# Kernel tuning notes

Measured on AMD Instinct MI355X. Metric: run time of the kernel, lower is better.

Reference implementation:

```python
import jax, jax.numpy as jnp
import numpy as np

N = 50000   # nodes
E = 800000  # edges per graph
FD = 128    # input feature dim (sc and fc)
H = 128     # hidden_dim
G = 64      # graphs in batch
C = 2       # num_classes


def _sage(x, src, dst, Wl, Wr, b, n):
    # PyG SAGEConv (mean aggr): lin_l(mean_{j->i} x_j) + lin_r(x_i); bias lives in lin_l.
    msum = jax.ops.segment_sum(x[src], dst, num_segments=n)          # [n, F]
    cnt = jax.ops.segment_sum(jnp.ones((src.shape[0],), x.dtype), dst, num_segments=n)
    mean = msum / jnp.maximum(cnt, 1.0)[:, None]
    return mean @ Wl.T + x @ Wr.T + b


def setup_inputs() -> dict:
    key = jax.random.key(0)
    ks = jax.random.split(key, 24)
    s = 0.05
    inp = {
        "sc_x": jax.random.normal(ks[0], (N, FD), jnp.float32),
        "fc_x": jax.random.normal(ks[1], (N, FD), jnp.float32),
        "sc_edge_index": jax.random.randint(ks[2], (2, E), 0, N),
        "fc_edge_index": jax.random.randint(ks[3], (2, E), 0, N),
        "batch": jnp.sort(jax.random.randint(ks[4], (N,), 0, G)),
        # sc convs
        "sc_Wl1": jax.random.normal(ks[5], (H, FD), jnp.float32) * s,
        "sc_Wr1": jax.random.normal(ks[6], (H, FD), jnp.float32) * s,
        "sc_b1": jnp.zeros((H,), jnp.float32),
        "sc_Wl2": jax.random.normal(ks[7], (H, H), jnp.float32) * s,
        "sc_Wr2": jax.random.normal(ks[8], (H, H), jnp.float32) * s,
        "sc_b2": jnp.zeros((H,), jnp.float32),
        # fc convs
        "fc_Wl1": jax.random.normal(ks[9], (H, FD), jnp.float32) * s,
        "fc_Wr1": jax.random.normal(ks[10], (H, FD), jnp.float32) * s,
        "fc_b1": jnp.zeros((H,), jnp.float32),
        "fc_Wl2": jax.random.normal(ks[11], (H, H), jnp.float32) * s,
        "fc_Wr2": jax.random.normal(ks[12], (H, H), jnp.float32) * s,
        "fc_b2": jnp.zeros((H,), jnp.float32),
        # MLP head
        "W1": jax.random.normal(ks[13], (H, 2 * H), jnp.float32) * s,
        "bh1": jnp.zeros((H,), jnp.float32),
        "W2": jax.random.normal(ks[14], (H // 2, H), jnp.float32) * s,
        "bh2": jnp.zeros((H // 2,), jnp.float32),
        "W3": jax.random.normal(ks[15], (C, H // 2), jnp.float32) * s,
        "bh3": jnp.zeros((C,), jnp.float32),
    }
    return inp


def reference(sc_x, fc_x, sc_edge_index, fc_edge_index, batch,
              sc_Wl1, sc_Wr1, sc_b1, sc_Wl2, sc_Wr2, sc_b2,
              fc_Wl1, fc_Wr1, fc_b1, fc_Wl2, fc_Wr2, fc_b2,
              W1, bh1, W2, bh2, W3, bh3):
    # edge_index[0] = source j, edge_index[1] = target i (PyG convention)
    sc_src, sc_dst = sc_edge_index[0], sc_edge_index[1]
    fc_src, fc_dst = fc_edge_index[0], fc_edge_index[1]

    h = jax.nn.relu(_sage(sc_x, sc_src, sc_dst, sc_Wl1, sc_Wr1, sc_b1, N))
    h = jax.nn.relu(_sage(h, sc_src, sc_dst, sc_Wl2, sc_Wr2, sc_b2, N))
    sc_pool = jax.ops.segment_sum(h, batch, num_segments=G)  # global_add_pool -> [G, H]

    g = jax.nn.relu(_sage(fc_x, fc_src, fc_dst, fc_Wl1, fc_Wr1, fc_b1, N))
    g = jax.nn.relu(_sage(g, fc_src, fc_dst, fc_Wl2, fc_Wr2, fc_b2, N))
    fc_pool = jax.ops.segment_sum(g, batch, num_segments=G)  # [G, H]

    x = jnp.concatenate([sc_pool, fc_pool], axis=1)          # [G, 2H]
    # dropout is identity in eval mode
    x = jax.nn.relu(x @ W1.T + bh1)
    x = jax.nn.relu(x @ W2.T + bh2)
    return jax.nn.log_softmax(x @ W3.T + bh3, axis=-1)       # [G, C]
```

## Files before the change

### kernel.cpp

```cpp
#include <hip/hip_runtime.h>
#include <hip/hip_bf16.h>

#define N_NODES 50000
#define E_EDGES 800000
#define G_GRAPHS 64
#define NBUCK 392
#define BCAP 5120
#define NF ((size_t)N_NODES * 128)

typedef __attribute__((ext_vector_type(8))) short s16x8;
typedef __attribute__((ext_vector_type(4))) float f32x4;

constexpr size_t O_POOL   = 0;
constexpr size_t O_GCUR   = 16384;
constexpr size_t O_BSTART = 16896;
constexpr size_t O_ROW    = 17408;
constexpr size_t O_CNT    = 117408;
constexpr size_t O_ES     = 217408;
constexpr size_t O_WB     = 1817408;
constexpr size_t O_XB     = 1882944;
constexpr size_t O_MEAN   = 8282944;
constexpr size_t O_HB     = 14682944;
constexpr size_t ZERO_BYTES = (16384 + 512) * 4;

__device__ __forceinline__ unsigned short f2bf(float f) {
    __hip_bfloat16 h = __float2bfloat16(f);
    return *reinterpret_cast<unsigned short*>(&h);
}
__device__ __forceinline__ float bflo(unsigned int v) { return __uint_as_float(v << 16); }
__device__ __forceinline__ float bfhi(unsigned int v) { return __uint_as_float(v & 0xffff0000u); }

__global__ void __launch_bounds__(512) bin_pass1(const int* __restrict__ sc_e,
                                                 const int* __restrict__ fc_e,
                                                 int* __restrict__ gcur,
                                                 unsigned int* __restrict__ buf) {
    __shared__ int hcnt[512];
    __shared__ int hexcl[512];
    __shared__ int hcur[512];
    __shared__ int gbase[512];
    __shared__ int wsum[8];
    __shared__ unsigned int stage[4096];

    const int tid = threadIdx.x;
    const int lane = tid & 63;
    const int wid = tid >> 6;
    const int tile0 = blockIdx.x * 4096;

    hcnt[tid] = 0;
    __syncthreads();

    int eb[8];
    unsigned int pk[8];
    #pragma unroll
    for (int j = 0; j < 8; ++j) {
        int ec = tile0 + j * 512 + tid;
        if (ec < 2 * E_EDGES) {
            int set = (ec >= E_EDGES);
            int local = ec - set * E_EDGES;
            const int* ep = set ? fc_e : sc_e;
            int src = ep[local];
            int dst = ep[E_EDGES + local];
            eb[j] = set * 196 + (dst >> 8);
            pk[j] = ((unsigned int)(dst & 255) << 16) | (unsigned int)src;
            atomicAdd(&hcnt[eb[j]], 1);
        } else eb[j] = -1;
    }
    __syncthreads();

    {
        int v = hcnt[tid];
        int incl = v;
        #pragma unroll
        for (int d = 1; d < 64; d <<= 1) {
            int u = __shfl_up(incl, d, 64);
            if (lane >= d) incl += u;
        }
        if (lane == 63) wsum[wid] = incl;
        __syncthreads();
        int pre = 0;
        for (int w = 0; w < wid; ++w) pre += wsum[w];
        int excl = incl - v + pre;
        hexcl[tid] = excl;
        hcur[tid] = excl;
    }
    __syncthreads();

    if (tid < NBUCK) {
        int c = hcnt[tid];
        gbase[tid] = c ? atomicAdd(&gcur[tid], c) : 0;
    }

    #pragma unroll
    for (int j = 0; j < 8; ++j) {
        if (eb[j] >= 0) {
            int pos = atomicAdd(&hcur[eb[j]], 1);
            stage[pos] = pk[j];
        }
    }
    __syncthreads();

    for (int b = wid; b < NBUCK; b += 8) {
        int c = hcnt[b];
        if (!c) continue;
        int s = hexcl[b];
        int g0 = gbase[b];
        for (int i = lane; i < c; i += 64) {
            int gi = g0 + i;
            if (gi < BCAP) buf[(size_t)b * BCAP + gi] = stage[s + i];
        }
    }
}

__global__ void bstart_scan(const int* __restrict__ gcur, int* __restrict__ bstart) {
    __shared__ int wsum[8];
    int t = threadIdx.x;
    int lane = t & 63, wid = t >> 6;
    int v = (t < NBUCK) ? min(gcur[t], BCAP) : 0;
    int incl = v;
    #pragma unroll
    for (int d = 1; d < 64; d <<= 1) {
        int u = __shfl_up(incl, d, 64);
        if (lane >= d) incl += u;
    }
    if (lane == 63) wsum[wid] = incl;
    __syncthreads();
    int pre = 0;
    for (int w = 0; w < wid; ++w) pre += wsum[w];
    if (t < NBUCK) bstart[t] = incl - v + pre;
}

__global__ void __launch_bounds__(256) bin_pass2(const unsigned int* __restrict__ buf,
                                                 const int* __restrict__ gcur,
                                                 const int* __restrict__ bstart,
                                                 int* __restrict__ row,
                                                 int* __restrict__ cnt,
                                                 int* __restrict__ es) {
    __shared__ int cntl[256];
    __shared__ int pexcl[256];
    __shared__ int pcur[256];
    __shared__ int wsum[4];
    __shared__ int stage[BCAP];

    const int b = blockIdx.x;
    const int tid = threadIdx.x;
    const int lane = tid & 63, wid = tid >> 6;
    const int sz = min(gcur[b], BCAP);
    const unsigned int* mybuf = buf + (size_t)b * BCAP;
    const int n0 = (b % 196) * 256;
    const int setbase = (b / 196) * N_NODES;

    cntl[tid] = 0;
    __syncthreads();
    for (int i = tid; i < sz; i += 256)
        atomicAdd(&cntl[mybuf[i] >> 16], 1);
    __syncthreads();
    {
        int v = cntl[tid];
        int incl = v;
        #pragma unroll
        for (int d = 1; d < 64; d <<= 1) {
            int u = __shfl_up(incl, d, 64);
            if (lane >= d) incl += u;
        }
        if (lane == 63) wsum[wid] = incl;
        __syncthreads();
        int pre = 0;
        for (int w = 0; w < wid; ++w) pre += wsum[w];
        int excl = incl - v + pre;
        pexcl[tid] = excl;
        pcur[tid] = excl;
    }
    __syncthreads();
    for (int i = tid; i < sz; i += 256) {
        unsigned int p = mybuf[i];
        int pos = atomicAdd(&pcur[p >> 16], 1);
        stage[pos] = (int)(p & 0xFFFFu);
    }
    __syncthreads();
    const int base = bstart[b];
    for (int i = tid; i < sz; i += 256) es[base + i] = stage[i];
    int node = n0 + tid;
    if (node < N_NODES) {
        cnt[setbase + node] = cntl[tid];
        row[setbase + node] = base + pexcl[tid];
    }
}

__global__ void cvt_w_kernel(const float* w0, const float* w1, const float* w2, const float* w3,
                             const float* w4, const float* w5, const float* w6, const float* w7,
                             unsigned short* __restrict__ wb) {
    const float* W;
    int m = blockIdx.y;
    switch (m) {
        case 0: W = w0; break; case 1: W = w1; break;
        case 2: W = w2; break; case 3: W = w3; break;
        case 4: W = w4; break; case 5: W = w5; break;
        case 6: W = w6; break; default: W = w7; break;
    }
    int i = blockIdx.x * 256 + threadIdx.x;
    wb[(size_t)m * 16384 + i] = f2bf(W[i]);
}

__global__ void cvt_x_kernel(const float* __restrict__ sc_x, const float* __restrict__ fc_x,
                             unsigned short* __restrict__ dst) {
    int i = blockIdx.x * 256 + threadIdx.x;
    if (i >= 2 * (N_NODES * 128) / 8) return;
    int set = (i >= (N_NODES * 128) / 8);
    int local = i - set * (N_NODES * 128) / 8;
    const float* src = set ? fc_x : sc_x;
    const float4* s = reinterpret_cast<const float4*>(src) + (size_t)local * 2;
    float4 a = s[0], b = s[1];
    union { s16x8 v; unsigned short u[8]; } p;
    p.u[0] = f2bf(a.x); p.u[1] = f2bf(a.y); p.u[2] = f2bf(a.z); p.u[3] = f2bf(a.w);
    p.u[4] = f2bf(b.x); p.u[5] = f2bf(b.y); p.u[6] = f2bf(b.z); p.u[7] = f2bf(b.w);
    reinterpret_cast<s16x8*>(dst)[i] = p.v;
}

__global__ void __launch_bounds__(256) agg_kernel(const unsigned short* __restrict__ x,
                                                  const int* __restrict__ row,
                                                  const int* __restrict__ cnt,
                                                  const int* __restrict__ es,
                                                  unsigned short* __restrict__ mean) {
    int wave = (blockIdx.x * 256 + threadIdx.x) >> 6;
    int lane = threadIdx.x & 63;
    int ql = lane & 15;
    int n = wave * 4 + (lane >> 4);
    if (n >= 2 * N_NODES) return;
    const unsigned short* xs = x + (n >= N_NODES ? NF : 0);
    int start = row[n];
    int deg = cnt[n];
    float a0 = 0.f, a1 = 0.f, a2 = 0.f, a3 = 0.f, a4 = 0.f, a5 = 0.f, a6 = 0.f, a7 = 0.f;
    int qbase = lane & 48;
    for (int c = 0; c < deg; c += 16) {
        int m = min(16, deg - c);
        int eid = (ql < m) ? es[start + c + ql] : 0;
        int j = 0;
        for (; j + 4 <= m; j += 4) {
            int s0 = __shfl(eid, qbase + j,     64);
            int s1 = __shfl(eid, qbase + j + 1, 64);
            int s2 = __shfl(eid, qbase + j + 2, 64);
            int s3 = __shfl(eid, qbase + j + 3, 64);
            uint4 v0 = *reinterpret_cast<const uint4*>(xs + (size_t)s0 * 128 + ql * 8);
            uint4 v1 = *reinterpret_cast<const uint4*>(xs + (size_t)s1 * 128 + ql * 8);
            uint4 v2 = *reinterpret_cast<const uint4*>(xs + (size_t)s2 * 128 + ql * 8);
            uint4 v3 = *reinterpret_cast<const uint4*>(xs + (size_t)s3 * 128 + ql * 8);
            a0 += bflo(v0.x) + bflo(v1.x) + bflo(v2.x) + bflo(v3.x);
            a1 += bfhi(v0.x) + bfhi(v1.x) + bfhi(v2.x) + bfhi(v3.x);
            a2 += bflo(v0.y) + bflo(v1.y) + bflo(v2.y) + bflo(v3.y);
            a3 += bfhi(v0.y) + bfhi(v1.y) + bfhi(v2.y) + bfhi(v3.y);
            a4 += bflo(v0.z) + bflo(v1.z) + bflo(v2.z) + bflo(v3.z);
            a5 += bfhi(v0.z) + bfhi(v1.z) + bfhi(v2.z) + bfhi(v3.z);
            a6 += bflo(v0.w) + bflo(v1.w) + bflo(v2.w) + bflo(v3.w);
            a7 += bfhi(v0.w) + bfhi(v1.w) + bfhi(v2.w) + bfhi(v3.w);
        }
        for (; j < m; ++j) {
            int s = __shfl(eid, qbase + j, 64);
            uint4 v = *reinterpret_cast<const uint4*>(xs + (size_t)s * 128 + ql * 8);
            a0 += bflo(v.x); a1 += bfhi(v.x);
            a2 += bflo(v.y); a3 += bfhi(v.y);
            a4 += bflo(v.z); a5 += bfhi(v.z);
            a6 += bflo(v.w); a7 += bfhi(v.w);
        }
    }
    float inv = 1.0f / fmaxf((float)deg, 1.0f);
    uint4 o;
    o.x = (unsigned int)f2bf(a0 * inv) | ((unsigned int)f2bf(a1 * inv) << 16);
    o.y = (unsigned int)f2bf(a2 * inv) | ((unsigned int)f2bf(a3 * inv) << 16);
    o.z = (unsigned int)f2bf(a4 * inv) | ((unsigned int)f2bf(a5 * inv) << 16);
    o.w = (unsigned int)f2bf(a6 * inv) | ((unsigned int)f2bf(a7 * inv) << 16);
    *reinterpret_cast<uint4*>(mean + (size_t)n * 128 + ql * 8) = o;
}

__global__ void __launch_bounds__(256) gemm_mfma(const unsigned short* __restrict__ AmB,
                                                 const unsigned short* __restrict__ AxB,
                                                 const unsigned short* __restrict__ WBall,
                                                 const float* __restrict__ bias0,
                                                 const float* __restrict__ bias1,
                                                 unsigned short* __restrict__ outHB,
                                                 float* __restrict__ pool,
                                                 const int* __restrict__ batch,
                                                 int layer) {
    __shared__ s16x8 lds_a[2][256];
    __shared__ s16x8 lds_b[2][512];

    const int tid = threadIdx.x;
    const int lane = tid & 63;
    const int w = tid >> 6;
    const int set = blockIdx.y;
    const int node0 = blockIdx.x * 64;

    const unsigned short* Am = AmB + (size_t)set * NF;
    const unsigned short* Ax = AxB + (size_t)set * NF;
    const unsigned short* Bl = WBall + (size_t)(set * 4 + layer * 2) * 16384;
    const unsigned short* Br = Bl + 16384;
    const float* bias = set ? bias1 : bias0;
    unsigned short* outH = outHB ? outHB + (size_t)set * NF : nullptr;
    const int poolBase = set * 128;

    const int wr = w >> 1;
    const int wc = w & 1;
    const int fr = lane & 15;
    const int fg = lane >> 4;

    f32x4 acc[2][4];
    #pragma unroll
    for (int mf = 0; mf < 2; ++mf)
        #pragma unroll
        for (int nf = 0; nf < 4; ++nf) acc[mf][nf] = (f32x4){0.f, 0.f, 0.f, 0.f};

    const int sa_row = tid >> 2, sa_slot = tid & 3;
    const int sa_g = sa_slot ^ ((sa_row >> 1) & 3);
    const size_t a_off = (size_t)min(node0 + sa_row, N_NODES - 1) * 128 + sa_g * 8;
    const int sb_row0 = tid >> 2;
    const size_t b_off0 = (size_t)sb_row0 * 128 + (sa_slot ^ ((sb_row0 >> 1) & 3)) * 8;
    const int sb_row1 = 64 + (tid >> 2);
    const size_t b_off1 = (size_t)sb_row1 * 128 + (sa_slot ^ ((sb_row1 >> 1) & 3)) * 8;

    const int arow0 = wr * 32 + fr;
    const int arow1 = arow0 + 16;
    const int aidx0 = arow0 * 4 + (fg ^ ((arow0 >> 1) & 3));
    const int aidx1 = arow1 * 4 + (fg ^ ((arow1 >> 1) & 3));
    int bidx[4];
    #pragma unroll
    for (int nf = 0; nf < 4; ++nf) {
        int br = wc * 64 + nf * 16 + fr;
        bidx[nf] = br * 4 + (fg ^ ((br >> 1) & 3));
    }

    #define LOAD_A(kc) (*reinterpret_cast<const s16x8*>(((kc) < 4 ? Am : Ax) + (((kc) & 3) * 32) + a_off))
    #define LOAD_B0(kc) (*reinterpret_cast<const s16x8*>(((kc) < 4 ? Bl : Br) + (((kc) & 3) * 32) + b_off0))
    #define LOAD_B1(kc) (*reinterpret_cast<const s16x8*>(((kc) < 4 ? Bl : Br) + (((kc) & 3) * 32) + b_off1))

    {
        s16x8 ra = LOAD_A(0), rb0 = LOAD_B0(0), rb1 = LOAD_B1(0);
        lds_a[0][tid] = ra; lds_b[0][tid] = rb0; lds_b[0][256 + tid] = rb1;
    }
    __syncthreads();

    #pragma unroll
    for (int kc = 0; kc < 8; ++kc) {
        const int cur = kc & 1;
        s16x8 ra, rb0, rb1;
        if (kc < 7) { ra = LOAD_A(kc + 1); rb0 = LOAD_B0(kc + 1); rb1 = LOAD_B1(kc + 1); }
        s16x8 a0 = lds_a[cur][aidx0];
        s16x8 a1 = lds_a[cur][aidx1];
        #pragma unroll
        for (int nf = 0; nf < 4; ++nf) {
            s16x8 bv = lds_b[cur][bidx[nf]];
            acc[0][nf] = __builtin_amdgcn_mfma_f32_16x16x32_bf16(a0, bv, acc[0][nf], 0, 0, 0);
            acc[1][nf] = __builtin_amdgcn_mfma_f32_16x16x32_bf16(a1, bv, acc[1][nf], 0, 0, 0);
        }
        if (kc < 7) { lds_a[cur ^ 1][tid] = ra; lds_b[cur ^ 1][tid] = rb0; lds_b[cur ^ 1][256 + tid] = rb1; }
        __syncthreads();
    }
    #undef LOAD_A
    #undef LOAD_B0
    #undef LOAD_B1

    if (outH) {
        #pragma unroll
        for (int mf = 0; mf < 2; ++mf)
            #pragma unroll
            for (int nf = 0; nf < 4; ++nf) {
                int col = wc * 64 + nf * 16 + fr;
                float bv = bias[col];
                #pragma unroll
                for (int r = 0; r < 4; ++r) {
                    int node = node0 + wr * 32 + mf * 16 + fg * 4 + r;
                    if (node < N_NODES)
                        outH[(size_t)node * 128 + col] = f2bf(fmaxf(acc[mf][nf][r] + bv, 0.f));
                }
            }
    } else {
        int gids[2][4];
        #pragma unroll
        for (int mf = 0; mf < 2; ++mf)
            #pragma unroll
            for (int r = 0; r < 4; ++r) {
                int node = node0 + wr * 32 + mf * 16 + fg * 4 + r;
                gids[mf][r] = (node < N_NODES) ? batch[node] : -1;
            }
        #pragma unroll
        for (int nf = 0; nf < 4; ++nf) {
            int col = wc * 64 + nf * 16 + fr;
            float bv = bias[col];
            float* pbase = &pool[poolBase + col];
            int curg = -1; float s = 0.f;
            #pragma unroll
            for (int mf = 0; mf < 2; ++mf)
                #pragma unroll
                for (int r = 0; r < 4; ++r) {
                    int g = gids[mf][r];
                    if (g < 0) continue;
                    float v = fmaxf(acc[mf][nf][r] + bv, 0.f);
                    if (g != curg) {
                        if (curg >= 0) atomicAdd(pbase + (size_t)curg * 256, s);
                        curg = g; s = v;
                    } else s += v;
                }
            if (curg >= 0) atomicAdd(pbase + (size_t)curg * 256, s);
        }
    }
}

__global__ void __launch_bounds__(128) head_kernel(const float* __restrict__ pool,
                                                   const float* __restrict__ W1, const float* __restrict__ bh1,
                                                   const float* __restrict__ W2, const float* __restrict__ bh2,
                                                   const float* __restrict__ W3, const float* __restrict__ bh3,
                                                   float* __restrict__ out) {
    __shared__ float xg[256];
    __shared__ float h1[128];
    __shared__ float h2[64];
    __shared__ float lg[2];
    int g = blockIdx.x, t = threadIdx.x;
    xg[t] = pool[(size_t)g * 256 + t];
    xg[t + 128] = pool[(size_t)g * 256 + 128 + t];
    __syncthreads();
    float s = bh1[t];
    for (int k = 0; k < 256; ++k) s += W1[t * 256 + k] * xg[k];
    h1[t] = fmaxf(s, 0.f);
    __syncthreads();
    if (t < 64) {
        float s2 = bh2[t];
        for (int k = 0; k < 128; ++k) s2 += W2[t * 128 + k] * h1[k];
        h2[t] = fmaxf(s2, 0.f);
    }
    __syncthreads();
    if (t < 2) {
        float s3 = bh3[t];
        for (int k = 0; k < 64; ++k) s3 += W3[t * 64 + k] * h2[k];
        lg[t] = s3;
    }
    __syncthreads();
    if (t == 0) {
        float m = fmaxf(lg[0], lg[1]);
        float lse = m + logf(expf(lg[0] - m) + expf(lg[1] - m));
        out[g * 2 + 0] = lg[0] - lse;
        out[g * 2 + 1] = lg[1] - lse;
    }
}

extern "C" void kernel_launch(void* const* d_in, const int* in_sizes, int n_in,
                              void* d_out, int out_size, void* d_ws, size_t ws_size,
                              hipStream_t stream) {
    const float* sc_x = (const float*)d_in[0];
    const float* fc_x = (const float*)d_in[1];
    const int* sc_e   = (const int*)d_in[2];
    const int* fc_e   = (const int*)d_in[3];
    const int* batch  = (const int*)d_in[4];
    const float* sc_Wl1 = (const float*)d_in[5];
    const float* sc_Wr1 = (const float*)d_in[6];
    const float* sc_b1  = (const float*)d_in[7];
    const float* sc_Wl2 = (const float*)d_in[8];
    const float* sc_Wr2 = (const float*)d_in[9];
    const float* sc_b2  = (const float*)d_in[10];
    const float* fc_Wl1 = (const float*)d_in[11];
    const float* fc_Wr1 = (const float*)d_in[12];
    const float* fc_b1  = (const float*)d_in[13];
    const float* fc_Wl2 = (const float*)d_in[14];
    const float* fc_Wr2 = (const float*)d_in[15];
    const float* fc_b2  = (const float*)d_in[16];
    const float* W1  = (const float*)d_in[17];
    const float* bh1 = (const float*)d_in[18];
    const float* W2  = (const float*)d_in[19];
    const float* bh2 = (const float*)d_in[20];
    const float* W3  = (const float*)d_in[21];
    const float* bh3 = (const float*)d_in[22];

    int* iw = (int*)d_ws;
    float* fw = (float*)d_ws;
    float* pool = fw + O_POOL;
    int* gcur   = iw + O_GCUR;
    int* bstart = iw + O_BSTART;
    int* row    = iw + O_ROW;
    int* cnt    = iw + O_CNT;
    int* es     = iw + O_ES;
    unsigned short* WB    = (unsigned short*)(iw + O_WB);
    unsigned short* xb    = (unsigned short*)(iw + O_XB);
    unsigned short* meanb = (unsigned short*)(iw + O_MEAN);
    unsigned short* hb    = (unsigned short*)(iw + O_HB);
    unsigned int* buf = (unsigned int*)(iw + O_MEAN);

    hipMemsetAsync(d_ws, 0, ZERO_BYTES, stream);

    bin_pass1<<<(2 * E_EDGES + 4095) / 4096, 512, 0, stream>>>(sc_e, fc_e, gcur, buf);
    bstart_scan<<<1, 512, 0, stream>>>(gcur, bstart);
    bin_pass2<<<NBUCK, 256, 0, stream>>>(buf, gcur, bstart, row, cnt, es);

    cvt_w_kernel<<<dim3(64, 8), 256, 0, stream>>>(sc_Wl1, sc_Wr1, sc_Wl2, sc_Wr2,
                                                  fc_Wl1, fc_Wr1, fc_Wl2, fc_Wr2, WB);
    cvt_x_kernel<<<2 * 3125, 256, 0, stream>>>(sc_x, fc_x, xb);

    const int AGB = (2 * N_NODES + 15) / 16;
    dim3 gg((N_NODES + 63) / 64, 2);

    agg_kernel<<<AGB, 256, 0, stream>>>(xb, row, cnt, es, meanb);
    gemm_mfma<<<gg, 256, 0, stream>>>(meanb, xb, WB, sc_b1, fc_b1, hb, nullptr, nullptr, 0);
    agg_kernel<<<AGB, 256, 0, stream>>>(hb, row, cnt, es, meanb);
    gemm_mfma<<<gg, 256, 0, stream>>>(meanb, hb, WB, sc_b2, fc_b2, nullptr, pool, batch, 1);

    head_kernel<<<G_GRAPHS, 128, 0, stream>>>(pool, W1, bh1, W2, bh2, W3, bh3, (float*)d_out);
}
```

Before: 351.5 us.

## Fold bucket scan into bin_pass2, merge conversions, widen GEMM tile to 128 rows

Each bin_pass2 block now recomputes the bucket-start prefix scan in shared memory, which removes the separate bstart_scan launch. The weight and feature bf16 conversion kernels are merged into one launch, and the weight path is vectorized to 8 elements per thread. The GEMM now uses 512-thread blocks covering 128 nodes, so each B tile is loaded once per 128 rows instead of per 64. The cost is a redundant 392-entry scan in every block, plus fewer, larger GEMM blocks that change occupancy and the partial-tile tail.

```diff
diff --git a/kernel.cpp b/kernel.cpp
--- a/kernel.cpp
+++ b/kernel.cpp
@@ -13,7 +13,6 @@
 
 constexpr size_t O_POOL   = 0;
 constexpr size_t O_GCUR   = 16384;
-constexpr size_t O_BSTART = 16896;
 constexpr size_t O_ROW    = 17408;
 constexpr size_t O_CNT    = 117408;
 constexpr size_t O_ES     = 217408;
@@ -111,27 +110,8 @@
     }
 }
 
-__global__ void bstart_scan(const int* __restrict__ gcur, int* __restrict__ bstart) {
-    __shared__ int wsum[8];
-    int t = threadIdx.x;
-    int lane = t & 63, wid = t >> 6;
-    int v = (t < NBUCK) ? min(gcur[t], BCAP) : 0;
-    int incl = v;
-    #pragma unroll
-    for (int d = 1; d < 64; d <<= 1) {
-        int u = __shfl_up(incl, d, 64);
-        if (lane >= d) incl += u;
-    }
-    if (lane == 63) wsum[wid] = incl;
-    __syncthreads();
-    int pre = 0;
-    for (int w = 0; w < wid; ++w) pre += wsum[w];
-    if (t < NBUCK) bstart[t] = incl - v + pre;
-}
-
 __global__ void __launch_bounds__(256) bin_pass2(const unsigned int* __restrict__ buf,
                                                  const int* __restrict__ gcur,
-                                                 const int* __restrict__ bstart,
                                                  int* __restrict__ row,
                                                  int* __restrict__ cnt,
                                                  int* __restrict__ es) {
@@ -139,6 +119,7 @@
     __shared__ int pexcl[256];
     __shared__ int pcur[256];
     __shared__ int wsum[4];
+    __shared__ int pre[512];
     __shared__ int stage[BCAP];
 
     const int b = blockIdx.x;
@@ -149,11 +130,30 @@
     const int n0 = (b % 196) * 256;
     const int setbase = (b / 196) * N_NODES;
 
+    pre[tid] = (tid < NBUCK) ? min(gcur[tid], BCAP) : 0;
+    if (tid + 256 < 512) pre[tid + 256] = (tid + 256 < NBUCK) ? min(gcur[tid + 256], BCAP) : 0;
     cntl[tid] = 0;
     __syncthreads();
+    if (tid < 64) {
+        int base = tid * 8;
+        int loc[8];
+        int s = 0;
+        #pragma unroll
+        for (int k = 0; k < 8; ++k) { loc[k] = s; s += pre[base + k]; }
+        int incl = s;
+        #pragma unroll
+        for (int d = 1; d < 64; d <<= 1) {
+            int u = __shfl_up(incl, d, 64);
+            if (lane >= d) incl += u;
+        }
+        int excl = incl - s;
+        #pragma unroll
+        for (int k = 0; k < 8; ++k) pre[base + k] = excl + loc[k];
+    }
     for (int i = tid; i < sz; i += 256)
         atomicAdd(&cntl[mybuf[i] >> 16], 1);
     __syncthreads();
+    const int base = pre[b];
     {
         int v = cntl[tid];
         int incl = v;
@@ -164,9 +164,9 @@
         }
         if (lane == 63) wsum[wid] = incl;
         __syncthreads();
-        int pre = 0;
-        for (int w = 0; w < wid; ++w) pre += wsum[w];
-        int excl = incl - v + pre;
+        int p = 0;
+        for (int w = 0; w < wid; ++w) p += wsum[w];
+        int excl = incl - v + p;
         pexcl[tid] = excl;
         pcur[tid] = excl;
     }
@@ -177,7 +177,6 @@
         stage[pos] = (int)(p & 0xFFFFu);
     }
     __syncthreads();
-    const int base = bstart[b];
     for (int i = tid; i < sz; i += 256) es[base + i] = stage[i];
     int node = n0 + tid;
     if (node < N_NODES) {
@@ -186,34 +185,42 @@
     }
 }
 
-__global__ void cvt_w_kernel(const float* w0, const float* w1, const float* w2, const float* w3,
-                             const float* w4, const float* w5, const float* w6, const float* w7,
-                             unsigned short* __restrict__ wb) {
-    const float* W;
-    int m = blockIdx.y;
-    switch (m) {
-        case 0: W = w0; break; case 1: W = w1; break;
-        case 2: W = w2; break; case 3: W = w3; break;
-        case 4: W = w4; break; case 5: W = w5; break;
-        case 6: W = w6; break; default: W = w7; break;
-    }
-    int i = blockIdx.x * 256 + threadIdx.x;
-    wb[(size_t)m * 16384 + i] = f2bf(W[i]);
-}
-
-__global__ void cvt_x_kernel(const float* __restrict__ sc_x, const float* __restrict__ fc_x,
-                             unsigned short* __restrict__ dst) {
-    int i = blockIdx.x * 256 + threadIdx.x;
-    if (i >= 2 * (N_NODES * 128) / 8) return;
-    int set = (i >= (N_NODES * 128) / 8);
-    int local = i - set * (N_NODES * 128) / 8;
-    const float* src = set ? fc_x : sc_x;
-    const float4* s = reinterpret_cast<const float4*>(src) + (size_t)local * 2;
-    float4 a = s[0], b = s[1];
-    union { s16x8 v; unsigned short u[8]; } p;
-    p.u[0] = f2bf(a.x); p.u[1] = f2bf(a.y); p.u[2] = f2bf(a.z); p.u[3] = f2bf(a.w);
-    p.u[4] = f2bf(b.x); p.u[5] = f2bf(b.y); p.u[6] = f2bf(b.z); p.u[7] = f2bf(b.w);
-    reinterpret_cast<s16x8*>(dst)[i] = p.v;
+__global__ void cvt_all(const float* __restrict__ sc_x, const float* __restrict__ fc_x,
+                        const float* w0, const float* w1, const float* w2, const float* w3,
+                        const float* w4, const float* w5, const float* w6, const float* w7,
+                        unsigned short* __restrict__ xb, unsigned short* __restrict__ wb) {
+    const int blk = blockIdx.x;
+    const int tid = threadIdx.x;
+    if (blk < 6250) {
+        int i = blk * 256 + tid;
+        int set = (i >= (N_NODES * 128) / 8);
+        int local = i - set * (N_NODES * 128) / 8;
+        const float* src = set ? fc_x : sc_x;
+        const float4* s = reinterpret_cast<const float4*>(src) + (size_t)local * 2;
+        float4 a = s[0], b = s[1];
+        union { s16x8 v; unsigned short u[8]; } p;
+        p.u[0] = f2bf(a.x); p.u[1] = f2bf(a.y); p.u[2] = f2bf(a.z); p.u[3] = f2bf(a.w);
+        p.u[4] = f2bf(b.x); p.u[5] = f2bf(b.y); p.u[6] = f2bf(b.z); p.u[7] = f2bf(b.w);
+        reinterpret_cast<s16x8*>(xb)[i] = p.v;
+    } else {
+        int widx = blk - 6250;
+        int gi = widx * 2048 + tid * 8;
+        int m = gi >> 14;
+        int off = gi & 16383;
+        const float* W;
+        switch (m) {
+            case 0: W = w0; break; case 1: W = w1; break;
+            case 2: W = w2; break; case 3: W = w3; break;
+            case 4: W = w4; break; case 5: W = w5; break;
+            case 6: W = w6; break; default: W = w7; break;
+        }
+        const float4* s = reinterpret_cast<const float4*>(W + off);
+        float4 a = s[0], b = s[1];
+        union { s16x8 v; unsigned short u[8]; } p;
+        p.u[0] = f2bf(a.x); p.u[1] = f2bf(a.y); p.u[2] = f2bf(a.z); p.u[3] = f2bf(a.w);
+        p.u[4] = f2bf(b.x); p.u[5] = f2bf(b.y); p.u[6] = f2bf(b.z); p.u[7] = f2bf(b.w);
+        *reinterpret_cast<s16x8*>(wb + gi) = p.v;
+    }
 }
 
 __global__ void __launch_bounds__(256) agg_kernel(const unsigned short* __restrict__ x,
@@ -271,7 +278,7 @@
     *reinterpret_cast<uint4*>(mean + (size_t)n * 128 + ql * 8) = o;
 }
 
-__global__ void __launch_bounds__(256) gemm_mfma(const unsigned short* __restrict__ AmB,
+__global__ void __launch_bounds__(512) gemm_mfma(const unsigned short* __restrict__ AmB,
                                                  const unsigned short* __restrict__ AxB,
                                                  const unsigned short* __restrict__ WBall,
                                                  const float* __restrict__ bias0,
@@ -280,14 +287,14 @@
                                                  float* __restrict__ pool,
                                                  const int* __restrict__ batch,
                                                  int layer) {
-    __shared__ s16x8 lds_a[2][256];
+    __shared__ s16x8 lds_a[2][512];
     __shared__ s16x8 lds_b[2][512];
 
     const int tid = threadIdx.x;
     const int lane = tid & 63;
     const int w = tid >> 6;
     const int set = blockIdx.y;
-    const int node0 = blockIdx.x * 64;
+    const int node0 = blockIdx.x * 128;
 
     const unsigned short* Am = AmB + (size_t)set * NF;
     const unsigned short* Ax = AxB + (size_t)set * NF;
@@ -308,13 +315,10 @@
         #pragma unroll
         for (int nf = 0; nf < 4; ++nf) acc[mf][nf] = (f32x4){0.f, 0.f, 0.f, 0.f};
 
-    const int sa_row = tid >> 2, sa_slot = tid & 3;
-    const int sa_g = sa_slot ^ ((sa_row >> 1) & 3);
-    const size_t a_off = (size_t)min(node0 + sa_row, N_NODES - 1) * 128 + sa_g * 8;
-    const int sb_row0 = tid >> 2;
-    const size_t b_off0 = (size_t)sb_row0 * 128 + (sa_slot ^ ((sb_row0 >> 1) & 3)) * 8;
-    const int sb_row1 = 64 + (tid >> 2);
-    const size_t b_off1 = (size_t)sb_row1 * 128 + (sa_slot ^ ((sb_row1 >> 1) & 3)) * 8;
+    const int s_row = tid >> 2, s_slot = tid & 3;
+    const int s_g = s_slot ^ ((s_row >> 1) & 3);
+    const size_t a_off = (size_t)min(node0 + s_row, N_NODES - 1) * 128 + s_g * 8;
+    const size_t b_off = (size_t)s_row * 128 + s_g * 8;
 
     const int arow0 = wr * 32 + fr;
     const int arow1 = arow0 + 16;
@@ -328,20 +332,19 @@
     }
 
     #define LOAD_A(kc) (*reinterpret_cast<const s16x8*>(((kc) < 4 ? Am : Ax) + (((kc) & 3) * 32) + a_off))
-    #define LOAD_B0(kc) (*reinterpret_cast<const s16x8*>(((kc) < 4 ? Bl : Br) + (((kc) & 3) * 32) + b_off0))
-    #define LOAD_B1(kc) (*reinterpret_cast<const s16x8*>(((kc) < 4 ? Bl : Br) + (((kc) & 3) * 32) + b_off1))
+    #define LOAD_B(kc) (*reinterpret_cast<const s16x8*>(((kc) < 4 ? Bl : Br) + (((kc) & 3) * 32) + b_off))
 
     {
-        s16x8 ra = LOAD_A(0), rb0 = LOAD_B0(0), rb1 = LOAD_B1(0);
-        lds_a[0][tid] = ra; lds_b[0][tid] = rb0; lds_b[0][256 + tid] = rb1;
+        s16x8 ra = LOAD_A(0), rb = LOAD_B(0);
+        lds_a[0][tid] = ra; lds_b[0][tid] = rb;
     }
     __syncthreads();
 
     #pragma unroll
     for (int kc = 0; kc < 8; ++kc) {
         const int cur = kc & 1;
-        s16x8 ra, rb0, rb1;
-        if (kc < 7) { ra = LOAD_A(kc + 1); rb0 = LOAD_B0(kc + 1); rb1 = LOAD_B1(kc + 1); }
+        s16x8 ra, rb;
+        if (kc < 7) { ra = LOAD_A(kc + 1); rb = LOAD_B(kc + 1); }
         s16x8 a0 = lds_a[cur][aidx0];
         s16x8 a1 = lds_a[cur][aidx1];
         #pragma unroll
@@ -350,12 +353,11 @@
             acc[0][nf] = __builtin_amdgcn_mfma_f32_16x16x32_bf16(a0, bv, acc[0][nf], 0, 0, 0);
             acc[1][nf] = __builtin_amdgcn_mfma_f32_16x16x32_bf16(a1, bv, acc[1][nf], 0, 0, 0);
         }
-        if (kc < 7) { lds_a[cur ^ 1][tid] = ra; lds_b[cur ^ 1][tid] = rb0; lds_b[cur ^ 1][256 + tid] = rb1; }
+        if (kc < 7) { lds_a[cur ^ 1][tid] = ra; lds_b[cur ^ 1][tid] = rb; }
         __syncthreads();
     }
     #undef LOAD_A
-    #undef LOAD_B0
-    #undef LOAD_B1
+    #undef LOAD_B
 
     if (outH) {
         #pragma unroll
@@ -471,7 +473,6 @@
     float* fw = (float*)d_ws;
     float* pool = fw + O_POOL;
     int* gcur   = iw + O_GCUR;
-    int* bstart = iw + O_BSTART;
     int* row    = iw + O_ROW;
     int* cnt    = iw + O_CNT;
     int* es     = iw + O_ES;
@@ -484,20 +485,19 @@
     hipMemsetAsync(d_ws, 0, ZERO_BYTES, stream);
 
     bin_pass1<<<(2 * E_EDGES + 4095) / 4096, 512, 0, stream>>>(sc_e, fc_e, gcur, buf);
-    bstart_scan<<<1, 512, 0, stream>>>(gcur, bstart);
-    bin_pass2<<<NBUCK, 256, 0, stream>>>(buf, gcur, bstart, row, cnt, es);
-
-    cvt_w_kernel<<<dim3(64, 8), 256, 0, stream>>>(sc_Wl1, sc_Wr1, sc_Wl2, sc_Wr2,
-                                                  fc_Wl1, fc_Wr1, fc_Wl2, fc_Wr2, WB);
-    cvt_x_kernel<<<2 * 3125, 256, 0, stream>>>(sc_x, fc_x, xb);
+    bin_pass2<<<NBUCK, 256, 0, stream>>>(buf, gcur, row, cnt, es);
+
+    cvt_all<<<6250 + 64, 256, 0, stream>>>(sc_x, fc_x,
+                                           sc_Wl1, sc_Wr1, sc_Wl2, sc_Wr2,
+                                           fc_Wl1, fc_Wr1, fc_Wl2, fc_Wr2, xb, WB);
 
     const int AGB = (2 * N_NODES + 15) / 16;
-    dim3 gg((N_NODES + 63) / 64, 2);
+    dim3 gg((N_NODES + 127) / 128, 2);
 
     agg_kernel<<<AGB, 256, 0, stream>>>(xb, row, cnt, es, meanb);
-    gemm_mfma<<<gg, 256, 0, stream>>>(meanb, xb, WB, sc_b1, fc_b1, hb, nullptr, nullptr, 0);
+    gemm_mfma<<<gg, 512, 0, stream>>>(meanb, xb, WB, sc_b1, fc_b1, hb, nullptr, nullptr, 0);
     agg_kernel<<<AGB, 256, 0, stream>>>(hb, row, cnt, es, meanb);
-    gemm_mfma<<<gg, 256, 0, stream>>>(meanb, hb, WB, sc_b2, fc_b2, nullptr, pool, batch, 1);
+    gemm_mfma<<<gg, 512, 0, stream>>>(meanb, hb, WB, sc_b2, fc_b2, nullptr, pool, batch, 1);
 
     head_kernel<<<G_GRAPHS, 128, 0, stream>>>(pool, W1, bh1, W2, bh2, W3, bh3, (float*)d_out);
 }
```

Result: faster. 342.7 us (-2.5%).
